# Kernel tuning notes

Hardware: AMD Instinct MI355X
Metric: run time of the kernel (lower is better)

The kernel has to match this reference:

```python
import jax, jax.numpy as jnp
import numpy as np

GAMMA = 1.5
BN_EPS = 1e-5


def sparsemax(z):
    """Sparsemax along last axis (Martins & Astudillo, 2016)."""
    z = z - jnp.max(z, axis=-1, keepdims=True)
    z_sorted = -jnp.sort(-z, axis=-1)                      # descending sort
    z_cumsum = jnp.cumsum(z_sorted, axis=-1)
    k = jnp.arange(1, z.shape[-1] + 1, dtype=z.dtype)
    support = (z_sorted - (z_cumsum - 1.0) / k) > 0
    k_z = jnp.clip(jnp.sum(support, axis=-1, keepdims=True), 1, None).astype(z.dtype)
    idx = (k_z - 1.0).astype(jnp.int32)
    tau = (jnp.take_along_axis(z_cumsum, idx, axis=-1) - 1.0) / k_z
    return jnp.clip(z - tau, 0.0, None)


def setup_inputs() -> dict:
    key = jax.random.key(0)
    k1, k2 = jax.random.split(key)
    B, T, E, H = 32, 512, 512, 8
    x = jax.random.normal(k1, (B, T, E), dtype=jnp.float32)
    # torch Linear weight (out, in), kaiming-ish scale
    W = jax.random.normal(k2, (H, E, E), dtype=jnp.float32) / np.float32(np.sqrt(E))
    bn_weight = jnp.ones((H, E), dtype=jnp.float32)
    bn_bias = jnp.zeros((H, E), dtype=jnp.float32)
    return {"x": x, "W": W, "bn_weight": bn_weight, "bn_bias": bn_bias}


def reference(x, W, bn_weight, bn_bias):
    B, T, E = x.shape
    H = W.shape[0]
    gi = x.reshape(B * T, E)
    # all-head linear: y[n,o] = sum_i gi[n,i] * W[h,o,i]
    logits = jnp.einsum('ni,hoi->hno', gi, W)              # (H, B*T, E)
    # BatchNorm1d in training mode: batch stats over the B*T axis, biased var
    mean = jnp.mean(logits, axis=1, keepdims=True)
    var = jnp.var(logits, axis=1, keepdims=True)
    logits = (logits - mean) / jnp.sqrt(var + BN_EPS)
    logits = logits * bn_weight[:, None, :] + bn_bias[:, None, :]
    logits = logits.reshape(H, B, T, E)

    prior0 = jnp.ones((B, T, E), dtype=x.dtype)

    def step(prior, logits_h):
        mask_h = sparsemax(logits_h * prior)
        prior = prior * jnp.clip(GAMMA - mask_h, 0.0, None)
        return prior, mask_h

    _, masks = jax.lax.scan(step, prior0, logits)          # masks: (H, B, T, E)
    masked_xs = x[None, :, :, :] * masks                   # (H, B, T, E)
    return masked_xs, jnp.transpose(masks, (1, 0, 2, 3))   # (B, H, T, E)
```

## Files before the change

### kernel.cpp

```cpp
#include <hip/hip_runtime.h>
#include <stdint.h>

#define Hh 8
#define Bb 32
#define Tt 512
#define Ee 512
#define Nn 16384
#define GAMMA_ 1.5f
#define BN_EPS_ 1e-5f

typedef _Float16 f16x4 __attribute__((ext_vector_type(4)));
typedef _Float16 f16x8 __attribute__((ext_vector_type(8)));
typedef float    f32x4 __attribute__((ext_vector_type(4)));

__device__ __forceinline__ void async_ld16(void* lds, const void* g) {
    __builtin_amdgcn_global_load_lds(
        (const __attribute__((address_space(1))) void*)g,
        (__attribute__((address_space(3))) void*)lds, 16, 0, 0);
}

__global__ __launch_bounds__(256) void cvt_kernel(const float* __restrict__ x,
                                                  const float* __restrict__ W,
                                                  _Float16* __restrict__ xh,
                                                  _Float16* __restrict__ wh) {
    const int NX = Bb * Tt * Ee;
    int i = (blockIdx.x * 256 + threadIdx.x) * 4;
    if (i < NX) {
        float4 v = *(const float4*)(x + i);
        f16x4 o = {(_Float16)v.x, (_Float16)v.y, (_Float16)v.z, (_Float16)v.w};
        *(f16x4*)(xh + i) = o;
    } else {
        int j = i - NX;
        float4 v = *(const float4*)(W + j);
        f16x4 o = {(_Float16)v.x, (_Float16)v.y, (_Float16)v.z, (_Float16)v.w};
        *(f16x4*)(wh + j) = o;
    }
}

__global__ __launch_bounds__(256) void gemm_kernel(const _Float16* __restrict__ A,
                                                   const _Float16* __restrict__ Bm,
                                                   _Float16* __restrict__ C,
                                                   float* __restrict__ sums,
                                                   float* __restrict__ sumsq) {
    __shared__ alignas(16) _Float16 As[128 * 32];
    __shared__ alignas(16) _Float16 Bs[128 * 32];
    const int h  = blockIdx.z;
    const int mb = blockIdx.x * 128;
    const int nb = blockIdx.y * 128;
    const int t    = threadIdx.x;
    const int lane = t & 63;
    const int w    = t >> 6;
    const int wm   = (w >> 1) * 64;
    const int wn   = (w & 1) * 64;
    const int quad = lane >> 4;
    const int l16  = lane & 15;

    const _Float16* Ap = A + (size_t)(mb + (t >> 2)) * Ee + (t & 3) * 8;
    const _Float16* Bp = Bm + (size_t)h * Ee * Ee + (size_t)(nb + (t >> 2)) * Ee + (t & 3) * 8;

    f32x4 acc[4][4] = {};

    for (int k0 = 0; k0 < Ee; k0 += 32) {
        async_ld16(&As[t * 8],        Ap + k0);
        async_ld16(&As[2048 + t * 8], Ap + 64 * Ee + k0);
        async_ld16(&Bs[t * 8],        Bp + k0);
        async_ld16(&Bs[2048 + t * 8], Bp + 64 * Ee + k0);
        __syncthreads();
        f16x8 a8[4], b8[4];
#pragma unroll
        for (int mt = 0; mt < 4; ++mt)
            a8[mt] = *(const f16x8*)(&As[(wm + mt * 16 + l16) * 32 + quad * 8]);
#pragma unroll
        for (int nt = 0; nt < 4; ++nt)
            b8[nt] = *(const f16x8*)(&Bs[(wn + nt * 16 + l16) * 32 + quad * 8]);
#pragma unroll
        for (int mt = 0; mt < 4; ++mt)
#pragma unroll
            for (int nt = 0; nt < 4; ++nt)
                acc[mt][nt] = __builtin_amdgcn_mfma_f32_16x16x32_f16(a8[mt], b8[nt], acc[mt][nt], 0, 0, 0);
        __syncthreads();
    }

#pragma unroll
    for (int nt = 0; nt < 4; ++nt) {
        float s = 0.f, ss = 0.f;
#pragma unroll
        for (int mt = 0; mt < 4; ++mt)
#pragma unroll
            for (int r = 0; r < 4; ++r) { float v = acc[mt][nt][r]; s += v; ss += v * v; }
        s  += __shfl_xor(s, 16, 64);  s  += __shfl_xor(s, 32, 64);
        ss += __shfl_xor(ss, 16, 64); ss += __shfl_xor(ss, 32, 64);
        if (quad == 0) {
            int col = nb + wn + nt * 16 + l16;
            atomicAdd(&sums[h * Ee + col], s);
            atomicAdd(&sumsq[h * Ee + col], ss);
        }
    }

    _Float16* Cp = C + (size_t)h * Nn * Ee;
#pragma unroll
    for (int mt = 0; mt < 4; ++mt)
#pragma unroll
        for (int r = 0; r < 4; ++r) {
            int row = mb + wm + mt * 16 + quad * 4 + r;
            size_t off = (size_t)row * Ee + nb + wn + l16;
#pragma unroll
            for (int nt = 0; nt < 4; ++nt)
                Cp[off + nt * 16] = (_Float16)acc[mt][nt][r];
        }
}

__global__ __launch_bounds__(256) void stats_kernel(const float* __restrict__ sums,
                                                    const float* __restrict__ sumsq,
                                                    const float* __restrict__ bnw,
                                                    const float* __restrict__ bnb,
                                                    float* __restrict__ cA,
                                                    float* __restrict__ cB) {
    int i = blockIdx.x * 256 + threadIdx.x;
    float mean = sums[i] * (1.0f / Nn);
    float var  = sumsq[i] * (1.0f / Nn) - mean * mean;
    float inv  = rsqrtf(var + BN_EPS_);
    float a    = bnw[i] * inv;
    cA[i] = a;
    cB[i] = bnb[i] - mean * a;
}

__global__ __launch_bounds__(256) void rows_kernel(const float* __restrict__ x,
                                                   const _Float16* __restrict__ lg,
                                                   const float* __restrict__ cA,
                                                   const float* __restrict__ cB,
                                                   float* __restrict__ out) {
    const int n    = blockIdx.x * 4 + (threadIdx.x >> 6);
    const int lane = threadIdx.x & 63;
    const int e0   = lane * 4;
    const int bb   = n >> 9;
    const int tt   = n & 511;

    float xr[8], prior[8], z[8], mk[8];
    {
        const float* xp = x + (size_t)n * Ee;
        float4 x0 = *(const float4*)(xp + e0);
        float4 x1 = *(const float4*)(xp + 256 + e0);
        xr[0]=x0.x; xr[1]=x0.y; xr[2]=x0.z; xr[3]=x0.w;
        xr[4]=x1.x; xr[5]=x1.y; xr[6]=x1.z; xr[7]=x1.w;
    }
#pragma unroll
    for (int j = 0; j < 8; ++j) prior[j] = 1.0f;

    float* omx = out;
    float* omk = out + (size_t)Hh * Nn * Ee;

    for (int h = 0; h < Hh; ++h) {
        const _Float16* lp = lg + (size_t)h * Nn * Ee + (size_t)n * Ee;
        f16x4 l0 = *(const f16x4*)(lp + e0);
        f16x4 l1 = *(const f16x4*)(lp + 256 + e0);
        const float* ap = cA + h * Ee;
        const float* bp = cB + h * Ee;
        float4 a0 = *(const float4*)(ap + e0);
        float4 a1 = *(const float4*)(ap + 256 + e0);
        float4 b0 = *(const float4*)(bp + e0);
        float4 b1 = *(const float4*)(bp + 256 + e0);
        float av[8] = {a0.x,a0.y,a0.z,a0.w,a1.x,a1.y,a1.z,a1.w};
        float bv[8] = {b0.x,b0.y,b0.z,b0.w,b1.x,b1.y,b1.z,b1.w};
        float lv[8] = {(float)l0[0],(float)l0[1],(float)l0[2],(float)l0[3],
                       (float)l1[0],(float)l1[1],(float)l1[2],(float)l1[3]};
#pragma unroll
        for (int j = 0; j < 8; ++j)
            z[j] = (lv[j] * av[j] + bv[j]) * prior[j];

        float tau = -1e30f;
        int cprev = -1;
        for (int it = 0; it < 600; ++it) {
            float s2 = 0.f, cf = 0.f;
#pragma unroll
            for (int j = 0; j < 8; ++j)
                if (z[j] > tau) { s2 += z[j]; cf += 1.0f; }
#pragma unroll
            for (int m = 32; m >= 1; m >>= 1) {
                s2 += __shfl_xor(s2, m, 64);
                cf += __shfl_xor(cf, m, 64);
            }
            int c = (int)cf;
            if (c == cprev) break;
            cprev = c;
            tau = (s2 - 1.0f) / cf;
        }

#pragma unroll
        for (int j = 0; j < 8; ++j) {
            mk[j] = fmaxf(z[j] - tau, 0.0f);
            prior[j] *= fmaxf(GAMMA_ - mk[j], 0.0f);
        }

        size_t oxoff = ((size_t)h * Nn + n) * Ee;
        size_t okoff = (((size_t)bb * Hh + h) * Tt + tt) * Ee;
        float4 vx0 = {xr[0]*mk[0], xr[1]*mk[1], xr[2]*mk[2], xr[3]*mk[3]};
        float4 vx1 = {xr[4]*mk[4], xr[5]*mk[5], xr[6]*mk[6], xr[7]*mk[7]};
        float4 vm0 = {mk[0], mk[1], mk[2], mk[3]};
        float4 vm1 = {mk[4], mk[5], mk[6], mk[7]};
        *(float4*)(omx + oxoff + e0)       = vx0;
        *(float4*)(omx + oxoff + 256 + e0) = vx1;
        *(float4*)(omk + okoff + e0)       = vm0;
        *(float4*)(omk + okoff + 256 + e0) = vm1;
    }
}

extern "C" void kernel_launch(void* const* d_in, const int* in_sizes, int n_in,
                              void* d_out, int out_size, void* d_ws, size_t ws_size,
                              hipStream_t stream) {
    const float* x   = (const float*)d_in[0];
    const float* W   = (const float*)d_in[1];
    const float* bnw = (const float*)d_in[2];
    const float* bnb = (const float*)d_in[3];
    float* out = (float*)d_out;

    uint8_t* ws = (uint8_t*)d_ws;
    _Float16* xh = (_Float16*)(ws);
    _Float16* wh = (_Float16*)(ws + 16777216);
    _Float16* lg = (_Float16*)(ws + 20971520);
    float* sums  = (float*)(ws + 155189248);
    float* sumsq = (float*)(ws + 155205632);
    float* cA    = (float*)(ws + 155222016);
    float* cB    = (float*)(ws + 155238400);

    hipMemsetAsync(sums, 0, 2 * 4096 * sizeof(float), stream);

    cvt_kernel<<<10240, 256, 0, stream>>>(x, W, xh, wh);
    gemm_kernel<<<dim3(128, 4, 8), 256, 0, stream>>>(xh, wh, lg, sums, sumsq);
    stats_kernel<<<16, 256, 0, stream>>>(sums, sumsq, bnw, bnb, cA, cB);
    rows_kernel<<<4096, 256, 0, stream>>>(x, lg, cA, cB, out);
}
```

Baseline: 749.3 us.

## Double-buffer GEMM LDS, prefetch logits, DPP reductions and nontemporal stores in sparsemax

The GEMM now double-buffers its LDS tiles and issues the next k-slice's async loads before computing the current one, which removes one barrier per iteration. The sparsemax kernel prefetches the next head's logits and replaces the shuffle reductions with DPP row operations plus readlane. It also seeds the threshold iteration with the mean and caps it at 64 iterations instead of 600, and writes outputs with nontemporal stores. The single barrier per GEMM iteration with async LDS loads risks a race, and the iteration cap could stop convergence early.

Result: faster. 676.0 us (-9.8%).

```diff
diff --git a/kernel.cpp b/kernel.cpp
--- a/kernel.cpp
+++ b/kernel.cpp
@@ -17,6 +17,23 @@
     __builtin_amdgcn_global_load_lds(
         (const __attribute__((address_space(1))) void*)g,
         (__attribute__((address_space(3))) void*)lds, 16, 0, 0);
+}
+
+__device__ __forceinline__ float dpp_sum64(float v) {
+    int t;
+    t = __builtin_amdgcn_update_dpp(0, __float_as_int(v), 0x111, 0xf, 0xf, true);
+    v += __int_as_float(t);
+    t = __builtin_amdgcn_update_dpp(0, __float_as_int(v), 0x112, 0xf, 0xf, true);
+    v += __int_as_float(t);
+    t = __builtin_amdgcn_update_dpp(0, __float_as_int(v), 0x114, 0xf, 0xf, true);
+    v += __int_as_float(t);
+    t = __builtin_amdgcn_update_dpp(0, __float_as_int(v), 0x118, 0xf, 0xf, true);
+    v += __int_as_float(t);
+    t = __builtin_amdgcn_update_dpp(0, __float_as_int(v), 0x142, 0xf, 0xf, true);
+    v += __int_as_float(t);
+    t = __builtin_amdgcn_update_dpp(0, __float_as_int(v), 0x143, 0xf, 0xf, true);
+    v += __int_as_float(t);
+    return __int_as_float(__builtin_amdgcn_readlane(__float_as_int(v), 63));
 }
 
 __global__ __launch_bounds__(256) void cvt_kernel(const float* __restrict__ x,
@@ -42,8 +59,8 @@
                                                    _Float16* __restrict__ C,
                                                    float* __restrict__ sums,
                                                    float* __restrict__ sumsq) {
-    __shared__ alignas(16) _Float16 As[128 * 32];
-    __shared__ alignas(16) _Float16 Bs[128 * 32];
+    __shared__ alignas(16) _Float16 As[2][128 * 32];
+    __shared__ alignas(16) _Float16 Bs[2][128 * 32];
     const int h  = blockIdx.z;
     const int mb = blockIdx.x * 128;
     const int nb = blockIdx.y * 128;
@@ -60,25 +77,34 @@
 
     f32x4 acc[4][4] = {};
 
+    async_ld16(&As[0][t * 8],        Ap);
+    async_ld16(&As[0][2048 + t * 8], Ap + 64 * Ee);
+    async_ld16(&Bs[0][t * 8],        Bp);
+    async_ld16(&Bs[0][2048 + t * 8], Bp + 64 * Ee);
+
+    int buf = 0;
     for (int k0 = 0; k0 < Ee; k0 += 32) {
-        async_ld16(&As[t * 8],        Ap + k0);
-        async_ld16(&As[2048 + t * 8], Ap + 64 * Ee + k0);
-        async_ld16(&Bs[t * 8],        Bp + k0);
-        async_ld16(&Bs[2048 + t * 8], Bp + 64 * Ee + k0);
         __syncthreads();
+        if (k0 + 32 < Ee) {
+            int nb2 = buf ^ 1;
+            async_ld16(&As[nb2][t * 8],        Ap + k0 + 32);
+            async_ld16(&As[nb2][2048 + t * 8], Ap + 64 * Ee + k0 + 32);
+            async_ld16(&Bs[nb2][t * 8],        Bp + k0 + 32);
+            async_ld16(&Bs[nb2][2048 + t * 8], Bp + 64 * Ee + k0 + 32);
+        }
         f16x8 a8[4], b8[4];
 #pragma unroll
         for (int mt = 0; mt < 4; ++mt)
-            a8[mt] = *(const f16x8*)(&As[(wm + mt * 16 + l16) * 32 + quad * 8]);
+            a8[mt] = *(const f16x8*)(&As[buf][(wm + mt * 16 + l16) * 32 + quad * 8]);
 #pragma unroll
         for (int nt = 0; nt < 4; ++nt)
-            b8[nt] = *(const f16x8*)(&Bs[(wn + nt * 16 + l16) * 32 + quad * 8]);
+            b8[nt] = *(const f16x8*)(&Bs[buf][(wn + nt * 16 + l16) * 32 + quad * 8]);
 #pragma unroll
         for (int mt = 0; mt < 4; ++mt)
 #pragma unroll
             for (int nt = 0; nt < 4; ++nt)
                 acc[mt][nt] = __builtin_amdgcn_mfma_f32_16x16x32_f16(a8[mt], b8[nt], acc[mt][nt], 0, 0, 0);
-        __syncthreads();
+        buf ^= 1;
     }
 
 #pragma unroll
@@ -150,10 +176,18 @@
     float* omx = out;
     float* omk = out + (size_t)Hh * Nn * Ee;
 
+    const _Float16* lp0 = lg + (size_t)n * Ee;
+    f16x4 l0 = *(const f16x4*)(lp0 + e0);
+    f16x4 l1 = *(const f16x4*)(lp0 + 256 + e0);
+
+#pragma unroll
     for (int h = 0; h < Hh; ++h) {
-        const _Float16* lp = lg + (size_t)h * Nn * Ee + (size_t)n * Ee;
-        f16x4 l0 = *(const f16x4*)(lp + e0);
-        f16x4 l1 = *(const f16x4*)(lp + 256 + e0);
+        f16x4 n0, n1;
+        if (h + 1 < Hh) {
+            const _Float16* lpn = lg + (size_t)(h + 1) * Nn * Ee + (size_t)n * Ee;
+            n0 = *(const f16x4*)(lpn + e0);
+            n1 = *(const f16x4*)(lpn + 256 + e0);
+        }
         const float* ap = cA + h * Ee;
         const float* bp = cB + h * Ee;
         float4 a0 = *(const float4*)(ap + e0);
@@ -168,22 +202,25 @@
         for (int j = 0; j < 8; ++j)
             z[j] = (lv[j] * av[j] + bv[j]) * prior[j];
 
-        float tau = -1e30f;
-        int cprev = -1;
-        for (int it = 0; it < 600; ++it) {
+        float sl = 0.f;
+#pragma unroll
+        for (int j = 0; j < 8; ++j) sl += z[j];
+        float tau = (dpp_sum64(sl) - 1.0f) * (1.0f / 512.0f);
+        int cprev = 512;
+        for (int it = 0; it < 64; ++it) {
             float s2 = 0.f, cf = 0.f;
 #pragma unroll
-            for (int j = 0; j < 8; ++j)
-                if (z[j] > tau) { s2 += z[j]; cf += 1.0f; }
-#pragma unroll
-            for (int m = 32; m >= 1; m >>= 1) {
-                s2 += __shfl_xor(s2, m, 64);
-                cf += __shfl_xor(cf, m, 64);
+            for (int j = 0; j < 8; ++j) {
+                bool p = z[j] > tau;
+                s2 += p ? z[j] : 0.0f;
+                cf += p ? 1.0f : 0.0f;
             }
-            int c = (int)cf;
+            float S = dpp_sum64(s2);
+            float Cc = dpp_sum64(cf);
+            int c = (int)Cc;
             if (c == cprev) break;
             cprev = c;
-            tau = (s2 - 1.0f) / cf;
+            tau = (S - 1.0f) / Cc;
         }
 
 #pragma unroll
@@ -194,14 +231,15 @@
 
         size_t oxoff = ((size_t)h * Nn + n) * Ee;
         size_t okoff = (((size_t)bb * Hh + h) * Tt + tt) * Ee;
-        float4 vx0 = {xr[0]*mk[0], xr[1]*mk[1], xr[2]*mk[2], xr[3]*mk[3]};
-        float4 vx1 = {xr[4]*mk[4], xr[5]*mk[5], xr[6]*mk[6], xr[7]*mk[7]};
-        float4 vm0 = {mk[0], mk[1], mk[2], mk[3]};
-        float4 vm1 = {mk[4], mk[5], mk[6], mk[7]};
-        *(float4*)(omx + oxoff + e0)       = vx0;
-        *(float4*)(omx + oxoff + 256 + e0) = vx1;
-        *(float4*)(omk + okoff + e0)       = vm0;
-        *(float4*)(omk + okoff + 256 + e0) = vm1;
+        f32x4 vx0 = {xr[0]*mk[0], xr[1]*mk[1], xr[2]*mk[2], xr[3]*mk[3]};
+        f32x4 vx1 = {xr[4]*mk[4], xr[5]*mk[5], xr[6]*mk[6], xr[7]*mk[7]};
+        f32x4 vm0 = {mk[0], mk[1], mk[2], mk[3]};
+        f32x4 vm1 = {mk[4], mk[5], mk[6], mk[7]};
+        __builtin_nontemporal_store(vx0, (f32x4*)(omx + oxoff + e0));
+        __builtin_nontemporal_store(vx1, (f32x4*)(omx + oxoff + 256 + e0));
+        __builtin_nontemporal_store(vm0, (f32x4*)(omk + okoff + e0));
+        __builtin_nontemporal_store(vm1, (f32x4*)(omk + okoff + 256 + e0));
+        l0 = n0; l1 = n1;
     }
 }
 
```
